# Kernel optimization log

Measured on AMD Instinct MI355X. Metric: run time of the kernel, lower is better.

Reference implementation:

```python
import jax, jax.numpy as jnp
import numpy as np

K = 3      # kernel_size
G = 2      # group
EPS = 1e-5 # BatchNorm eps


def setup_inputs() -> dict:
    key = jax.random.key(0)
    ks = jax.random.split(key, 6)
    n, c, h, w = 8, 256, 128, 128
    x = jax.random.normal(ks[0], (n, c, h, w), jnp.float32)
    conv_w = jax.random.normal(ks[1], (G * K * K, c, K, K), jnp.float32) * 0.02
    gamma = 1.0 + 0.1 * jax.random.normal(ks[2], (G * K * K,), jnp.float32)
    beta = 0.1 * jax.random.normal(ks[3], (G * K * K,), jnp.float32)
    run_mean = 0.1 * jax.random.normal(ks[4], (G * K * K,), jnp.float32)
    run_var = jax.random.uniform(ks[5], (G * K * K,), jnp.float32, 0.5, 1.5)
    return {"x": x, "conv_w": conv_w, "gamma": gamma, "beta": beta,
            "run_mean": run_mean, "run_var": run_var}


def reference(x, conv_w, gamma, beta, run_mean, run_var):
    n, c, h, w = x.shape
    p = K // 2
    # reflect pad, then VALID conv == 'same' spatial output
    xp = jnp.pad(x, ((0, 0), (0, 0), (p, p), (p, p)), mode='reflect')
    sigma = jax.lax.conv_general_dilated(
        xp, conv_w, window_strides=(1, 1), padding='VALID',
        dimension_numbers=('NCHW', 'OIHW', 'NCHW'))  # (n, G*K*K, h, w)
    # BatchNorm (eval mode: running stats)
    scale = gamma * jax.lax.rsqrt(run_var + EPS)
    sigma = sigma * scale[None, :, None, None] + (beta - run_mean * scale)[None, :, None, None]
    # softmax over ALL G*K*K channels (as in the original: softmax(dim=1))
    sigma = jax.nn.softmax(sigma, axis=1)
    # channel order is g*K*K + kk -> (n, G, K*K, h*w)
    sigma = sigma.reshape(n, G, K * K, h * w)
    # unfold: patches ordered (c, kh, kw) along feature dim, same as F.unfold
    patches = jax.lax.conv_general_dilated_patches(
        xp, filter_shape=(K, K), window_strides=(1, 1), padding='VALID',
        dimension_numbers=('NCHW', 'OIHW', 'NCHW'))  # (n, c*K*K, h, w)
    patches = patches.reshape(n, G, c // G, K * K, h * w)
    # per-pixel dynamic pooling: weighted sum over the K*K window
    out = jnp.einsum('ngckq,ngkq->ngcq', patches, sigma)
    return out.reshape(n, c, h, w)
```

## Files before the change

kernel.cpp:

```cpp
#include <hip/hip_runtime.h>
#include <cstdint>

#define HW  128
#define NCH 256
#define NOC 18
#define PLANE (HW * HW)
#define EPSBN 1e-5f

typedef __attribute__((ext_vector_type(8)))  short bf16x8;
typedef __attribute__((ext_vector_type(16))) float f32x16;

__device__ __forceinline__ unsigned short f2bf(float f) {
    union { float f; uint32_t u; } c; c.f = f;
    uint32_t u = c.u;
    uint32_t r = u + 0x7FFFu + ((u >> 16) & 1u);
    return (unsigned short)(r >> 16);
}

__device__ __forceinline__ int4 pack8(const float* v) {
    int4 d;
    d.x = (uint32_t)f2bf(v[0]) | ((uint32_t)f2bf(v[1]) << 16);
    d.y = (uint32_t)f2bf(v[2]) | ((uint32_t)f2bf(v[3]) << 16);
    d.z = (uint32_t)f2bf(v[4]) | ((uint32_t)f2bf(v[5]) << 16);
    d.w = (uint32_t)f2bf(v[6]) | ((uint32_t)f2bf(v[7]) << 16);
    return d;
}

__device__ __forceinline__ int lds_off(int buf, int slot, int px, int ic) {
    int b = ((((buf << 2) + slot) * 130 + px) * 32 + ic) * 2;
    return b ^ ((px & 6) << 3);
}

__global__ __launch_bounds__(256) void pasa_wprep(
    const float* __restrict__ w, unsigned short* __restrict__ wB)
{
    int idx = blockIdx.x * 256 + threadIdx.x;
    int icl = idx & 7;
    int oc  = (idx >> 3) & 31;
    int icb = (idx >> 8) & 31;
    int tap = idx >> 13;
    int ic  = icb * 8 + icl;
    float v = (oc < NOC) ? w[((size_t)oc * NCH + ic) * 9 + tap] : 0.0f;
    wB[idx] = f2bf(v);
}

__global__ __launch_bounds__(512, 4) void pasa_conv_mfma(
    const float* __restrict__ x, const unsigned short* __restrict__ wB,
    const float* __restrict__ gamma, const float* __restrict__ beta,
    const float* __restrict__ rmean, const float* __restrict__ rvar,
    float* __restrict__ sigma)
{
    __shared__ __align__(16) char lds[2 * 4 * 130 * 32 * 2];

    int flat = blockIdx.x;
    int nf   = (flat & 7) * 64 + (flat >> 3);
    const int n  = nf >> 6;
    const int y0 = (nf & 63) * 2;

    const int tid  = threadIdx.x;
    const int lane = tid & 63;
    const int wv   = tid >> 6;
    const int m    = lane & 31;
    const int hi   = lane >> 5;

    const int team = tid >> 7;
    const int p128 = tid & 127;
    int grow;
    if      (team == 0) grow = (y0 == 0) ? 1 : y0 - 1;
    else if (team == 1) grow = y0;
    else if (team == 2) grow = y0 + 1;
    else                grow = (y0 + 1 == HW - 1) ? HW - 2 : y0 + 2;

    const float* xrow = x + (size_t)n * NCH * PLANE + (size_t)grow * HW;

    const int out_row = wv >> 2;
    const int px_tile = (wv & 3) * 32;

    f32x16 acc;
    #pragma unroll
    for (int i = 0; i < 16; ++i) acc[i] = 0.0f;

    {
        float s0[8], s1[8], s2[8], s3[8];
        #pragma unroll
        for (int i = 0; i < 8; ++i) s0[i] = xrow[(size_t)(i)      * PLANE + p128];
        #pragma unroll
        for (int i = 0; i < 8; ++i) s1[i] = xrow[(size_t)(8 + i)  * PLANE + p128];
        #pragma unroll
        for (int i = 0; i < 8; ++i) s2[i] = xrow[(size_t)(16 + i) * PLANE + p128];
        #pragma unroll
        for (int i = 0; i < 8; ++i) s3[i] = xrow[(size_t)(24 + i) * PLANE + p128];
        int4 d0 = pack8(s0), d1 = pack8(s1), d2 = pack8(s2), d3 = pack8(s3);
        *(int4*)(lds + lds_off(0, team, p128 + 1, 0))  = d0;
        *(int4*)(lds + lds_off(0, team, p128 + 1, 8))  = d1;
        *(int4*)(lds + lds_off(0, team, p128 + 1, 16)) = d2;
        *(int4*)(lds + lds_off(0, team, p128 + 1, 24)) = d3;
        if (p128 == 1) {
            *(int4*)(lds + lds_off(0, team, 0, 0))  = d0;
            *(int4*)(lds + lds_off(0, team, 0, 8))  = d1;
            *(int4*)(lds + lds_off(0, team, 0, 16)) = d2;
            *(int4*)(lds + lds_off(0, team, 0, 24)) = d3;
        }
        if (p128 == 126) {
            *(int4*)(lds + lds_off(0, team, 129, 0))  = d0;
            *(int4*)(lds + lds_off(0, team, 129, 8))  = d1;
            *(int4*)(lds + lds_off(0, team, 129, 16)) = d2;
            *(int4*)(lds + lds_off(0, team, 129, 24)) = d3;
        }
    }
    __syncthreads();

    for (int c = 0; c < 8; ++c) {
        const int cb = c & 1;
        const bool more = (c < 7);
        float s0[8], s1[8], s2[8], s3[8];
        if (more) {
            const int icg = (c + 1) * 32;
            #pragma unroll
            for (int i = 0; i < 8; ++i) s0[i] = xrow[(size_t)(icg + i)      * PLANE + p128];
            #pragma unroll
            for (int i = 0; i < 8; ++i) s1[i] = xrow[(size_t)(icg + 8 + i)  * PLANE + p128];
            #pragma unroll
            for (int i = 0; i < 8; ++i) s2[i] = xrow[(size_t)(icg + 16 + i) * PLANE + p128];
            #pragma unroll
            for (int i = 0; i < 8; ++i) s3[i] = xrow[(size_t)(icg + 24 + i) * PLANE + p128];
        }
        #pragma unroll
        for (int tap = 0; tap < 9; ++tap) {
            const int dy = tap / 3;
            const int dx = tap % 3 - 1;
            const int slot = out_row + dy;
            const int apx  = px_tile + m + 1 + dx;
            #pragma unroll
            for (int ks = 0; ks < 2; ++ks) {
                bf16x8 a = *(const bf16x8*)(lds + lds_off(cb, slot, apx, ks * 16 + hi * 8));
                bf16x8 b = *(const bf16x8*)(wB +
                    (((size_t)tap * 32 + c * 4 + ks * 2 + hi) * 32 + m) * 8);
                acc = __builtin_amdgcn_mfma_f32_32x32x16_bf16(b, a, acc, 0, 0, 0);
            }
        }
        if (more) {
            const int tb = cb ^ 1;
            int4 d0 = pack8(s0), d1 = pack8(s1), d2 = pack8(s2), d3 = pack8(s3);
            *(int4*)(lds + lds_off(tb, team, p128 + 1, 0))  = d0;
            *(int4*)(lds + lds_off(tb, team, p128 + 1, 8))  = d1;
            *(int4*)(lds + lds_off(tb, team, p128 + 1, 16)) = d2;
            *(int4*)(lds + lds_off(tb, team, p128 + 1, 24)) = d3;
            if (p128 == 1) {
                *(int4*)(lds + lds_off(tb, team, 0, 0))  = d0;
                *(int4*)(lds + lds_off(tb, team, 0, 8))  = d1;
                *(int4*)(lds + lds_off(tb, team, 0, 16)) = d2;
                *(int4*)(lds + lds_off(tb, team, 0, 24)) = d3;
            }
            if (p128 == 126) {
                *(int4*)(lds + lds_off(tb, team, 129, 0))  = d0;
                *(int4*)(lds + lds_off(tb, team, 129, 8))  = d1;
                *(int4*)(lds + lds_off(tb, team, 129, 16)) = d2;
                *(int4*)(lds + lds_off(tb, team, 129, 24)) = d3;
            }
        }
        __syncthreads();
    }

    float vals[16];
    float mx = -3.0e38f;
    #pragma unroll
    for (int r = 0; r < 16; ++r) {
        int oc = (r & 3) + 8 * (r >> 2) + 4 * hi;
        float v = -3.0e38f;
        if (oc < NOC) {
            float sc = gamma[oc] * rsqrtf(rvar[oc] + EPSBN);
            float b  = beta[oc] - rmean[oc] * sc;
            v = fmaf(acc[r], sc, b);
        }
        vals[r] = v;
        mx = fmaxf(mx, v);
    }
    mx = fmaxf(mx, __shfl_xor(mx, 32));
    float s = 0.0f;
    #pragma unroll
    for (int r = 0; r < 16; ++r) {
        int oc = (r & 3) + 8 * (r >> 2) + 4 * hi;
        float e = (oc < NOC) ? __expf(vals[r] - mx) : 0.0f;
        vals[r] = e;
        s += e;
    }
    s += __shfl_xor(s, 32);
    const float inv = 1.0f / s;

    float* so = sigma + (size_t)n * NOC * PLANE
              + (size_t)(y0 + out_row) * HW + px_tile + m;
    #pragma unroll
    for (int r = 0; r < 16; ++r) {
        int oc = (r & 3) + 8 * (r >> 2) + 4 * hi;
        if (oc < NOC) so[(size_t)oc * PLANE] = vals[r] * inv;
    }
}

__global__ __launch_bounds__(256, 4) void pasa_pool(
    const float* __restrict__ x, const float* __restrict__ sigma,
    float* __restrict__ out)
{
    int flat = blockIdx.x;
    int nf   = (flat & 7) * 256 + (flat >> 3);
    const int n  = nf >> 8;
    const int cs = nf & 15;
    const int yt = (nf >> 4) & 15;

    const int lane = threadIdx.x & 63;
    const int col  = lane & 31;
    const int rs   = threadIdx.x >> 5;

    const int y   = yt * 8 + rs;
    const int px0 = col * 4;
    const int ym  = (y == 0)      ? 1      : y - 1;
    const int yp  = (y == HW - 1) ? HW - 2 : y + 1;
    const int g   = cs >> 3;

    const float* sg = sigma + ((size_t)n * NOC + g * 9) * PLANE
                            + (size_t)y * HW + px0;
    float sgv[9][4];
    #pragma unroll
    for (int k = 0; k < 9; ++k) {
        float4 t = *(const float4*)(sg + (size_t)k * PLANE);
        sgv[k][0] = t.x; sgv[k][1] = t.y; sgv[k][2] = t.z; sgv[k][3] = t.w;
    }

    const int c0 = cs * 16;
    const float* xn = x + (size_t)n * NCH * PLANE;
    float*       on = out + (size_t)n * NCH * PLANE;

    const size_t ymO = (size_t)ym * HW + px0;
    const size_t yO  = (size_t)y  * HW + px0;
    const size_t ypO = (size_t)yp * HW + px0;

    for (int cc = 0; cc < 16; ++cc) {
        const int c = c0 + cc;
        const float* xc = xn + (size_t)c * PLANE;
        float4 a = *(const float4*)(xc + ymO);
        float4 b = *(const float4*)(xc + yO);
        float4 d = *(const float4*)(xc + ypO);

        float la = __shfl(a.w, lane - 1); if (col == 0)  la = a.y;
        float lb = __shfl(b.w, lane - 1); if (col == 0)  lb = b.y;
        float ld = __shfl(d.w, lane - 1); if (col == 0)  ld = d.y;
        float ra = __shfl(a.x, lane + 1); if (col == 31) ra = a.z;
        float rb = __shfl(b.x, lane + 1); if (col == 31) rb = b.z;
        float rd = __shfl(d.x, lane + 1); if (col == 31) rd = d.z;

        float ov[4] = {0.f, 0.f, 0.f, 0.f};
        {
            float wv[6] = { la, a.x, a.y, a.z, a.w, ra };
            #pragma unroll
            for (int j = 0; j < 4; ++j)
                #pragma unroll
                for (int dx = 0; dx < 3; ++dx)
                    ov[j] = fmaf(wv[j + dx], sgv[dx][j], ov[j]);
        }
        {
            float wv[6] = { lb, b.x, b.y, b.z, b.w, rb };
            #pragma unroll
            for (int j = 0; j < 4; ++j)
                #pragma unroll
                for (int dx = 0; dx < 3; ++dx)
                    ov[j] = fmaf(wv[j + dx], sgv[3 + dx][j], ov[j]);
        }
        {
            float wv[6] = { ld, d.x, d.y, d.z, d.w, rd };
            #pragma unroll
            for (int j = 0; j < 4; ++j)
                #pragma unroll
                for (int dx = 0; dx < 3; ++dx)
                    ov[j] = fmaf(wv[j + dx], sgv[6 + dx][j], ov[j]);
        }
        float4 o4 = { ov[0], ov[1], ov[2], ov[3] };
        *(float4*)(on + (size_t)c * PLANE + yO) = o4;
    }
}

extern "C" void kernel_launch(void* const* d_in, const int* in_sizes, int n_in,
                              void* d_out, int out_size, void* d_ws, size_t ws_size,
                              hipStream_t stream) {
    const float* x     = (const float*)d_in[0];
    const float* w     = (const float*)d_in[1];
    const float* gamma = (const float*)d_in[2];
    const float* beta  = (const float*)d_in[3];
    const float* rmean = (const float*)d_in[4];
    const float* rvar  = (const float*)d_in[5];
    float* out   = (float*)d_out;
    float* sigma = (float*)d_ws;

    unsigned short* wB = (unsigned short*)(out + (size_t)16 * 1024 * 1024);

    pasa_wprep<<<dim3(288), dim3(256), 0, stream>>>(w, wB);
    pasa_conv_mfma<<<dim3(512), dim3(512), 0, stream>>>(
        x, wB, gamma, beta, rmean, rvar, sigma);
    pasa_pool<<<dim3(2048), dim3(256), 0, stream>>>(x, sigma, out);
}
```

Measured before the change: 111.0 us.

## Split conv tile into half-row-width blocks with 256 threads and explicit halo loads

The conv kernel now covers 2 output rows by 64 pixels per block instead of 2 rows by 128, doubling the grid to 1024 blocks of 256 threads. Each wave stages one input row into a smaller LDS buffer, and lanes fetch the left and right halo columns with extra scalar loads, applying reflect padding at the image edges. The goal is more blocks per CU and better load balance across the GPU. The cost is halo columns loaded twice and more weight-fragment reads per output.

Result: slower. 196.1 us (+76.7%).

```diff
diff --git a/kernel.cpp b/kernel.cpp
--- a/kernel.cpp
+++ b/kernel.cpp
@@ -27,7 +27,7 @@
 }
 
 __device__ __forceinline__ int lds_off(int buf, int slot, int px, int ic) {
-    int b = ((((buf << 2) + slot) * 130 + px) * 32 + ic) * 2;
+    int b = ((((buf << 2) + slot) * 66 + px) * 32 + ic) * 2;
     return b ^ ((px & 6) << 3);
 }
 
@@ -44,18 +44,20 @@
     wB[idx] = f2bf(v);
 }
 
-__global__ __launch_bounds__(512, 4) void pasa_conv_mfma(
+__global__ __launch_bounds__(256, 4) void pasa_conv_mfma(
     const float* __restrict__ x, const unsigned short* __restrict__ wB,
     const float* __restrict__ gamma, const float* __restrict__ beta,
     const float* __restrict__ rmean, const float* __restrict__ rvar,
     float* __restrict__ sigma)
 {
-    __shared__ __align__(16) char lds[2 * 4 * 130 * 32 * 2];
+    __shared__ __align__(16) char lds[2 * 4 * 66 * 32 * 2];
 
     int flat = blockIdx.x;
-    int nf   = (flat & 7) * 64 + (flat >> 3);
-    const int n  = nf >> 6;
-    const int y0 = (nf & 63) * 2;
+    int nf   = (flat & 7) * 128 + (flat >> 3);
+    const int n   = nf >> 7;
+    const int rem = nf & 127;
+    const int y0  = (rem >> 1) * 2;
+    const int P0  = (rem & 1) * 64;
 
     const int tid  = threadIdx.x;
     const int lane = tid & 63;
@@ -63,18 +65,21 @@
     const int m    = lane & 31;
     const int hi   = lane >> 5;
 
-    const int team = tid >> 7;
-    const int p128 = tid & 127;
     int grow;
-    if      (team == 0) grow = (y0 == 0) ? 1 : y0 - 1;
-    else if (team == 1) grow = y0;
-    else if (team == 2) grow = y0 + 1;
-    else                grow = (y0 + 1 == HW - 1) ? HW - 2 : y0 + 2;
-
-    const float* xrow = x + (size_t)n * NCH * PLANE + (size_t)grow * HW;
-
-    const int out_row = wv >> 2;
-    const int px_tile = (wv & 3) * 32;
+    if      (wv == 0) grow = (y0 == 0) ? 1 : y0 - 1;
+    else if (wv == 1) grow = y0;
+    else if (wv == 2) grow = y0 + 1;
+    else              grow = (y0 + 1 == HW - 1) ? HW - 2 : y0 + 2;
+
+    const float* xrow  = x + (size_t)n * NCH * PLANE + (size_t)grow * HW;
+    const int   gmain  = P0 + lane;
+    const int   hgpx   = (lane < 32) ? ((P0 == 0)  ? 1   : P0 - 1)
+                                     : ((P0 == 64) ? 126 : P0 + 64);
+    const int   hslot  = (lane < 32) ? 0 : 65;
+    const int   hic    = lane & 31;
+
+    const int out_row = wv >> 1;
+    const int px_t    = (wv & 1) * 32;
 
     f32x16 acc;
     #pragma unroll
@@ -83,54 +88,44 @@
     {
         float s0[8], s1[8], s2[8], s3[8];
         #pragma unroll
-        for (int i = 0; i < 8; ++i) s0[i] = xrow[(size_t)(i)      * PLANE + p128];
-        #pragma unroll
-        for (int i = 0; i < 8; ++i) s1[i] = xrow[(size_t)(8 + i)  * PLANE + p128];
-        #pragma unroll
-        for (int i = 0; i < 8; ++i) s2[i] = xrow[(size_t)(16 + i) * PLANE + p128];
-        #pragma unroll
-        for (int i = 0; i < 8; ++i) s3[i] = xrow[(size_t)(24 + i) * PLANE + p128];
-        int4 d0 = pack8(s0), d1 = pack8(s1), d2 = pack8(s2), d3 = pack8(s3);
-        *(int4*)(lds + lds_off(0, team, p128 + 1, 0))  = d0;
-        *(int4*)(lds + lds_off(0, team, p128 + 1, 8))  = d1;
-        *(int4*)(lds + lds_off(0, team, p128 + 1, 16)) = d2;
-        *(int4*)(lds + lds_off(0, team, p128 + 1, 24)) = d3;
-        if (p128 == 1) {
-            *(int4*)(lds + lds_off(0, team, 0, 0))  = d0;
-            *(int4*)(lds + lds_off(0, team, 0, 8))  = d1;
-            *(int4*)(lds + lds_off(0, team, 0, 16)) = d2;
-            *(int4*)(lds + lds_off(0, team, 0, 24)) = d3;
-        }
-        if (p128 == 126) {
-            *(int4*)(lds + lds_off(0, team, 129, 0))  = d0;
-            *(int4*)(lds + lds_off(0, team, 129, 8))  = d1;
-            *(int4*)(lds + lds_off(0, team, 129, 16)) = d2;
-            *(int4*)(lds + lds_off(0, team, 129, 24)) = d3;
-        }
+        for (int i = 0; i < 8; ++i) s0[i] = xrow[(size_t)(i)      * PLANE + gmain];
+        #pragma unroll
+        for (int i = 0; i < 8; ++i) s1[i] = xrow[(size_t)(8 + i)  * PLANE + gmain];
+        #pragma unroll
+        for (int i = 0; i < 8; ++i) s2[i] = xrow[(size_t)(16 + i) * PLANE + gmain];
+        #pragma unroll
+        for (int i = 0; i < 8; ++i) s3[i] = xrow[(size_t)(24 + i) * PLANE + gmain];
+        float hv = xrow[(size_t)hic * PLANE + hgpx];
+        *(int4*)(lds + lds_off(0, wv, lane + 1, 0))  = pack8(s0);
+        *(int4*)(lds + lds_off(0, wv, lane + 1, 8))  = pack8(s1);
+        *(int4*)(lds + lds_off(0, wv, lane + 1, 16)) = pack8(s2);
+        *(int4*)(lds + lds_off(0, wv, lane + 1, 24)) = pack8(s3);
+        *(unsigned short*)(lds + lds_off(0, wv, hslot, hic)) = f2bf(hv);
     }
     __syncthreads();
 
     for (int c = 0; c < 8; ++c) {
         const int cb = c & 1;
         const bool more = (c < 7);
-        float s0[8], s1[8], s2[8], s3[8];
+        float s0[8], s1[8], s2[8], s3[8], hv = 0.0f;
         if (more) {
             const int icg = (c + 1) * 32;
             #pragma unroll
-            for (int i = 0; i < 8; ++i) s0[i] = xrow[(size_t)(icg + i)      * PLANE + p128];
-            #pragma unroll
-            for (int i = 0; i < 8; ++i) s1[i] = xrow[(size_t)(icg + 8 + i)  * PLANE + p128];
-            #pragma unroll
-            for (int i = 0; i < 8; ++i) s2[i] = xrow[(size_t)(icg + 16 + i) * PLANE + p128];
-            #pragma unroll
-            for (int i = 0; i < 8; ++i) s3[i] = xrow[(size_t)(icg + 24 + i) * PLANE + p128];
+            for (int i = 0; i < 8; ++i) s0[i] = xrow[(size_t)(icg + i)      * PLANE + gmain];
+            #pragma unroll
+            for (int i = 0; i < 8; ++i) s1[i] = xrow[(size_t)(icg + 8 + i)  * PLANE + gmain];
+            #pragma unroll
+            for (int i = 0; i < 8; ++i) s2[i] = xrow[(size_t)(icg + 16 + i) * PLANE + gmain];
+            #pragma unroll
+            for (int i = 0; i < 8; ++i) s3[i] = xrow[(size_t)(icg + 24 + i) * PLANE + gmain];
+            hv = xrow[(size_t)(icg + hic) * PLANE + hgpx];
         }
         #pragma unroll
         for (int tap = 0; tap < 9; ++tap) {
             const int dy = tap / 3;
             const int dx = tap % 3 - 1;
             const int slot = out_row + dy;
-            const int apx  = px_tile + m + 1 + dx;
+            const int apx  = px_t + m + 1 + dx;
             #pragma unroll
             for (int ks = 0; ks < 2; ++ks) {
                 bf16x8 a = *(const bf16x8*)(lds + lds_off(cb, slot, apx, ks * 16 + hi * 8));
@@ -141,23 +136,11 @@
         }
         if (more) {
             const int tb = cb ^ 1;
-            int4 d0 = pack8(s0), d1 = pack8(s1), d2 = pack8(s2), d3 = pack8(s3);
-            *(int4*)(lds + lds_off(tb, team, p128 + 1, 0))  = d0;
-            *(int4*)(lds + lds_off(tb, team, p128 + 1, 8))  = d1;
-            *(int4*)(lds + lds_off(tb, team, p128 + 1, 16)) = d2;
-            *(int4*)(lds + lds_off(tb, team, p128 + 1, 24)) = d3;
-            if (p128 == 1) {
-                *(int4*)(lds + lds_off(tb, team, 0, 0))  = d0;
-                *(int4*)(lds + lds_off(tb, team, 0, 8))  = d1;
-                *(int4*)(lds + lds_off(tb, team, 0, 16)) = d2;
-                *(int4*)(lds + lds_off(tb, team, 0, 24)) = d3;
-            }
-            if (p128 == 126) {
-                *(int4*)(lds + lds_off(tb, team, 129, 0))  = d0;
-                *(int4*)(lds + lds_off(tb, team, 129, 8))  = d1;
-                *(int4*)(lds + lds_off(tb, team, 129, 16)) = d2;
-                *(int4*)(lds + lds_off(tb, team, 129, 24)) = d3;
-            }
+            *(int4*)(lds + lds_off(tb, wv, lane + 1, 0))  = pack8(s0);
+            *(int4*)(lds + lds_off(tb, wv, lane + 1, 8))  = pack8(s1);
+            *(int4*)(lds + lds_off(tb, wv, lane + 1, 16)) = pack8(s2);
+            *(int4*)(lds + lds_off(tb, wv, lane + 1, 24)) = pack8(s3);
+            *(unsigned short*)(lds + lds_off(tb, wv, hslot, hic)) = f2bf(hv);
         }
         __syncthreads();
     }
@@ -189,7 +172,7 @@
     const float inv = 1.0f / s;
 
     float* so = sigma + (size_t)n * NOC * PLANE
-              + (size_t)(y0 + out_row) * HW + px_tile + m;
+              + (size_t)(y0 + out_row) * HW + P0 + px_t + m;
     #pragma unroll
     for (int r = 0; r < 16; ++r) {
         int oc = (r & 3) + 8 * (r >> 2) + 4 * hi;
@@ -293,7 +276,7 @@
     unsigned short* wB = (unsigned short*)(out + (size_t)16 * 1024 * 1024);
 
     pasa_wprep<<<dim3(288), dim3(256), 0, stream>>>(w, wB);
-    pasa_conv_mfma<<<dim3(512), dim3(512), 0, stream>>>(
+    pasa_conv_mfma<<<dim3(1024), dim3(256), 0, stream>>>(
         x, wB, gamma, beta, rmean, rvar, sigma);
     pasa_pool<<<dim3(2048), dim3(256), 0, stream>>>(x, sigma, out);
 }
```

## Split conv input channels into two halves with a separate reduce-softmax kernel

Applied to the files above, without the earlier changes.

The conv kernel now splits the 256 input channels into two halves, launching 1024 blocks instead of 512 to raise parallelism on the device. Each block writes raw partial accumulators into scratch space inside the output buffer. A new kernel sums the two partials, then applies BatchNorm and softmax before writing sigma. This adds an extra launch plus global write and read traffic for the partials (2x18 planes per image) in exchange for better occupancy and shorter per-block latency.

Measured after the change: 103.0 us. 1.08x faster.

```diff
diff --git a/kernel.cpp b/kernel.cpp
--- a/kernel.cpp
+++ b/kernel.cpp
@@ -44,18 +44,17 @@
     wB[idx] = f2bf(v);
 }
 
-__global__ __launch_bounds__(512, 4) void pasa_conv_mfma(
+__global__ __launch_bounds__(512, 4) void pasa_conv_part(
     const float* __restrict__ x, const unsigned short* __restrict__ wB,
-    const float* __restrict__ gamma, const float* __restrict__ beta,
-    const float* __restrict__ rmean, const float* __restrict__ rvar,
-    float* __restrict__ sigma)
+    float* __restrict__ partial)
 {
     __shared__ __align__(16) char lds[2 * 4 * 130 * 32 * 2];
 
     int flat = blockIdx.x;
-    int nf   = (flat & 7) * 64 + (flat >> 3);
-    const int n  = nf >> 6;
-    const int y0 = (nf & 63) * 2;
+    const int n     = flat & 7;
+    const int local = flat >> 3;
+    const int h     = local >> 6;
+    const int y0    = (local & 63) * 2;
 
     const int tid  = threadIdx.x;
     const int lane = tid & 63;
@@ -71,7 +70,8 @@
     else if (team == 2) grow = y0 + 1;
     else                grow = (y0 + 1 == HW - 1) ? HW - 2 : y0 + 2;
 
-    const float* xrow = x + (size_t)n * NCH * PLANE + (size_t)grow * HW;
+    const float* xrow = x + (size_t)n * NCH * PLANE
+                      + (size_t)(h * 128) * PLANE + (size_t)grow * HW;
 
     const int out_row = wv >> 2;
     const int px_tile = (wv & 3) * 32;
@@ -110,9 +110,9 @@
     }
     __syncthreads();
 
-    for (int c = 0; c < 8; ++c) {
+    for (int c = 0; c < 4; ++c) {
         const int cb = c & 1;
-        const bool more = (c < 7);
+        const bool more = (c < 3);
         float s0[8], s1[8], s2[8], s3[8];
         if (more) {
             const int icg = (c + 1) * 32;
@@ -135,7 +135,7 @@
             for (int ks = 0; ks < 2; ++ks) {
                 bf16x8 a = *(const bf16x8*)(lds + lds_off(cb, slot, apx, ks * 16 + hi * 8));
                 bf16x8 b = *(const bf16x8*)(wB +
-                    (((size_t)tap * 32 + c * 4 + ks * 2 + hi) * 32 + m) * 8);
+                    (((size_t)tap * 32 + h * 16 + c * 4 + ks * 2 + hi) * 32 + m) * 8);
                 acc = __builtin_amdgcn_mfma_f32_32x32x16_bf16(b, a, acc, 0, 0, 0);
             }
         }
@@ -162,39 +162,51 @@
         __syncthreads();
     }
 
-    float vals[16];
-    float mx = -3.0e38f;
+    float* po = partial + ((size_t)(h * 8 + n) * NOC) * PLANE
+              + (size_t)(y0 + out_row) * HW + px_tile + m;
     #pragma unroll
     for (int r = 0; r < 16; ++r) {
         int oc = (r & 3) + 8 * (r >> 2) + 4 * hi;
-        float v = -3.0e38f;
-        if (oc < NOC) {
-            float sc = gamma[oc] * rsqrtf(rvar[oc] + EPSBN);
-            float b  = beta[oc] - rmean[oc] * sc;
-            v = fmaf(acc[r], sc, b);
-        }
-        vals[r] = v;
-        mx = fmaxf(mx, v);
-    }
-    mx = fmaxf(mx, __shfl_xor(mx, 32));
-    float s = 0.0f;
-    #pragma unroll
-    for (int r = 0; r < 16; ++r) {
-        int oc = (r & 3) + 8 * (r >> 2) + 4 * hi;
-        float e = (oc < NOC) ? __expf(vals[r] - mx) : 0.0f;
-        vals[r] = e;
-        s += e;
-    }
-    s += __shfl_xor(s, 32);
-    const float inv = 1.0f / s;
-
-    float* so = sigma + (size_t)n * NOC * PLANE
-              + (size_t)(y0 + out_row) * HW + px_tile + m;
-    #pragma unroll
-    for (int r = 0; r < 16; ++r) {
-        int oc = (r & 3) + 8 * (r >> 2) + 4 * hi;
-        if (oc < NOC) so[(size_t)oc * PLANE] = vals[r] * inv;
-    }
+        if (oc < NOC) po[(size_t)oc * PLANE] = acc[r];
+    }
+}
+
+__global__ __launch_bounds__(128) void pasa_reduce_softmax(
+    const float* __restrict__ partial,
+    const float* __restrict__ gamma, const float* __restrict__ beta,
+    const float* __restrict__ rmean, const float* __restrict__ rvar,
+    float* __restrict__ sigma)
+{
+    int flat = blockIdx.x;
+    int nf   = (flat & 7) * 128 + (flat >> 3);
+    const int n = nf >> 7;
+    const int y = nf & 127;
+    const int px = threadIdx.x;
+
+    const size_t off = (size_t)y * HW + px;
+    const float* p0 = partial + ((size_t)n * NOC) * PLANE + off;
+    const float* p1 = partial + ((size_t)(8 + n) * NOC) * PLANE + off;
+
+    float vals[NOC];
+    float mx = -3.0e38f;
+    #pragma unroll
+    for (int oc = 0; oc < NOC; ++oc) {
+        float s  = p0[(size_t)oc * PLANE] + p1[(size_t)oc * PLANE];
+        float sc = gamma[oc] * rsqrtf(rvar[oc] + EPSBN);
+        float b  = beta[oc] - rmean[oc] * sc;
+        float t  = fmaf(s, sc, b);
+        vals[oc] = t;
+        mx = fmaxf(mx, t);
+    }
+    float ssum = 0.0f;
+    #pragma unroll
+    for (int oc = 0; oc < NOC; ++oc) { vals[oc] = __expf(vals[oc] - mx); ssum += vals[oc]; }
+    const float inv = 1.0f / ssum;
+
+    float* so = sigma + (size_t)n * NOC * PLANE + off;
+    #pragma unroll
+    for (int oc = 0; oc < NOC; ++oc)
+        so[(size_t)oc * PLANE] = vals[oc] * inv;
 }
 
 __global__ __launch_bounds__(256, 4) void pasa_pool(
@@ -290,10 +302,12 @@
     float* out   = (float*)d_out;
     float* sigma = (float*)d_ws;
 
+    float* partial = out;
     unsigned short* wB = (unsigned short*)(out + (size_t)16 * 1024 * 1024);
 
     pasa_wprep<<<dim3(288), dim3(256), 0, stream>>>(w, wB);
-    pasa_conv_mfma<<<dim3(512), dim3(512), 0, stream>>>(
-        x, wB, gamma, beta, rmean, rvar, sigma);
+    pasa_conv_part<<<dim3(1024), dim3(512), 0, stream>>>(x, wB, partial);
+    pasa_reduce_softmax<<<dim3(1024), dim3(128), 0, stream>>>(
+        partial, gamma, beta, rmean, rvar, sigma);
     pasa_pool<<<dim3(2048), dim3(256), 0, stream>>>(x, sigma, out);
 }
```
